# Performance work log

Hardware: AMD Instinct MI355X
Metric: run time of the kernel (lower is better)

Reference implementation:

```python
import jax, jax.numpy as jnp
import numpy as np

D_MODEL = 1024
N_HEADS = 16
D_K = D_MODEL // N_HEADS
D_FF = 4096
EPS = 1e-6


def setup_inputs() -> dict:
    key = jax.random.key(0)
    ks = jax.random.split(key, 12)
    s = 1.0 / np.sqrt(D_MODEL)
    inp = {
        "x": jax.random.normal(ks[0], (4, 2048, D_MODEL), jnp.float32),
        "src_mask": jnp.ones((4, 1, 1, 2048), jnp.int32),
        "Wq": jax.random.normal(ks[1], (D_MODEL, D_MODEL), jnp.float32) * s,
        "bq": jnp.zeros((D_MODEL,), jnp.float32),
        "Wk": jax.random.normal(ks[2], (D_MODEL, D_MODEL), jnp.float32) * s,
        "bk": jnp.zeros((D_MODEL,), jnp.float32),
        "Wv": jax.random.normal(ks[3], (D_MODEL, D_MODEL), jnp.float32) * s,
        "bv": jnp.zeros((D_MODEL,), jnp.float32),
        "Wo": jax.random.normal(ks[4], (D_MODEL, D_MODEL), jnp.float32) * s,
        "bo": jnp.zeros((D_MODEL,), jnp.float32),
        "W1": jax.random.normal(ks[5], (D_MODEL, D_FF), jnp.float32) * s,
        "b1": jnp.zeros((D_FF,), jnp.float32),
        "W2": jax.random.normal(ks[6], (D_FF, D_MODEL), jnp.float32) * (1.0 / np.sqrt(D_FF)),
        "b2": jnp.zeros((D_MODEL,), jnp.float32),
        # scalar LayerNormalization params (alpha=ones(1), bias=zeros(1)) for the 2 residual norms
        "ln1_alpha": jnp.ones((1,), jnp.float32),
        "ln1_bias": jnp.zeros((1,), jnp.float32),
        "ln2_alpha": jnp.ones((1,), jnp.float32),
        "ln2_bias": jnp.zeros((1,), jnp.float32),
    }
    return inp


def _layernorm(x, alpha, bias):
    # matches torch: mean + std (unbiased, ddof=1), (x-mean)/(std+eps)
    mean = jnp.mean(x, axis=-1, keepdims=True)
    std = jnp.std(x, axis=-1, keepdims=True, ddof=1)
    return alpha * ((x - mean) / (std + EPS)) + bias


def _mha(x, mask, Wq, bq, Wk, bk, Wv, bv, Wo, bo):
    B, S, _ = x.shape
    q = (x @ Wq + bq).reshape(B, S, N_HEADS, D_K).transpose(0, 2, 1, 3)
    k = (x @ Wk + bk).reshape(B, S, N_HEADS, D_K).transpose(0, 2, 1, 3)
    v = (x @ Wv + bv).reshape(B, S, N_HEADS, D_K).transpose(0, 2, 1, 3)
    scores = jnp.einsum("bhqd,bhkd->bhqk", q, k) / jnp.sqrt(jnp.float32(D_K))
    scores = jnp.where(mask == 0, jnp.float32(-1e9), scores)
    attn = jax.nn.softmax(scores, axis=-1)
    ctx = jnp.einsum("bhqk,bhkd->bhqd", attn, v)
    ctx = ctx.transpose(0, 2, 1, 3).reshape(B, S, D_MODEL)
    return ctx @ Wo + bo


def reference(x, src_mask, Wq, bq, Wk, bk, Wv, bv, Wo, bo, W1, b1, W2, b2,
              ln1_alpha, ln1_bias, ln2_alpha, ln2_bias):
    # pre-norm residual 1: self-attention
    h = _layernorm(x, ln1_alpha, ln1_bias)
    x = x + _mha(h, src_mask, Wq, bq, Wk, bk, Wv, bv, Wo, bo)
    # pre-norm residual 2: FFN
    h = _layernorm(x, ln2_alpha, ln2_bias)
    ff = jax.nn.relu(h @ W1 + b1) @ W2 + b2
    return x + ff
```

## Files before the change

### kernel.cpp

```cpp
#include <hip/hip_runtime.h>

typedef __attribute__((ext_vector_type(8))) short v8s;
typedef __attribute__((ext_vector_type(8))) unsigned short v8u;
typedef __attribute__((ext_vector_type(4))) unsigned short v4u;
typedef __attribute__((ext_vector_type(4))) float f32x4;

#define DEV __device__ __forceinline__

DEV unsigned short f2bf(float f) {
  union { float f; unsigned u; } v; v.f = f;
  unsigned r = v.u + 0x7fffu + ((v.u >> 16) & 1u);
  return (unsigned short)(r >> 16);
}

DEV float bf2f(unsigned short s) {
  union { unsigned u; float f; } v; v.u = ((unsigned)s) << 16; return v.f;
}

DEV float fexp2(float x) {
  float r; asm("v_exp_f32 %0, %1" : "=v"(r) : "v"(x)); return r;
}

DEV void gload16(const unsigned short* g, unsigned short* l) {
  __builtin_amdgcn_global_load_lds(
      (const __attribute__((address_space(1))) unsigned int*)g,
      (__attribute__((address_space(3))) unsigned int*)l, 16, 0, 0);
}

#define SL2E 0.1803368801111204f

__global__ __launch_bounds__(256) void ln_kernel(
    const float* __restrict__ x, unsigned short* __restrict__ h,
    const float* __restrict__ alpha, const float* __restrict__ beta)
{
  int row = blockIdx.x;
  int tid = threadIdx.x;
  const float4* xr = reinterpret_cast<const float4*>(x + (size_t)row * 1024);
  float4 v = xr[tid];
  float s  = v.x + v.y + v.z + v.w;
  float ss = v.x * v.x + v.y * v.y + v.z * v.z + v.w * v.w;
#pragma unroll
  for (int off = 1; off < 64; off <<= 1) {
    s  += __shfl_xor(s, off);
    ss += __shfl_xor(ss, off);
  }
  __shared__ float ps[4][2];
  int wid = tid >> 6, lane = tid & 63;
  if (lane == 0) { ps[wid][0] = s; ps[wid][1] = ss; }
  __syncthreads();
  s  = ps[0][0] + ps[1][0] + ps[2][0] + ps[3][0];
  ss = ps[0][1] + ps[1][1] + ps[2][1] + ps[3][1];
  float mean = s * (1.0f / 1024.0f);
  float var  = (ss - 1024.0f * mean * mean) * (1.0f / 1023.0f);
  float inv  = 1.0f / (sqrtf(fmaxf(var, 0.0f)) + 1e-6f);
  float a = alpha[0], b = beta[0];
  v4u o;
  o[0] = f2bf(a * ((v.x - mean) * inv) + b);
  o[1] = f2bf(a * ((v.y - mean) * inv) + b);
  o[2] = f2bf(a * ((v.z - mean) * inv) + b);
  o[3] = f2bf(a * ((v.w - mean) * inv) + b);
  *reinterpret_cast<v4u*>(h + (size_t)row * 1024 + tid * 4) = o;
}

__global__ __launch_bounds__(256) void transpose_convert(
    const float* __restrict__ W, unsigned short* __restrict__ Wt, int K, int N)
{
  __shared__ float t[32][33];
  int n0 = blockIdx.x * 32, k0 = blockIdx.y * 32;
  int tx = threadIdx.x, ty = threadIdx.y;
#pragma unroll
  for (int i = 0; i < 4; ++i)
    t[ty + i * 8][tx] = W[(size_t)(k0 + ty + i * 8) * N + n0 + tx];
  __syncthreads();
#pragma unroll
  for (int i = 0; i < 4; ++i)
    Wt[(size_t)(n0 + ty + i * 8) * K + k0 + tx] = f2bf(t[tx][ty + i * 8]);
}

enum { MODE_QKV = 0, MODE_FFN1 = 3, MODE_PART = 4 };

template <int MODE>
__global__ __launch_bounds__(512, 1) void gemm_256s(
    const unsigned short* __restrict__ A, const unsigned short* __restrict__ Bt,
    const float* __restrict__ bias0, const float* __restrict__ bias1,
    const float* __restrict__ bias2,
    void* __restrict__ o0, void* __restrict__ o1, void* __restrict__ o2,
    int M, int N, int K, int KRUN)
{
  __shared__ unsigned short lds[2][512 * 64];

  int nbx = M >> 8, nwg = gridDim.x;
  int lin = blockIdx.x;
  int qq = nwg >> 3, rr = nwg & 7;
  int xcd = lin & 7, idx = lin >> 3;
  int swz = (xcd < rr ? xcd * (qq + 1) : rr * (qq + 1) + (xcd - rr) * qq) + idx;

  int bx, by, kbase;
  if constexpr (MODE == MODE_PART) {
    int h = swz >> 7, s2 = swz & 127;
    bx = s2 % nbx; by = s2 / nbx; kbase = h * KRUN;
  } else {
    bx = swz % nbx; by = swz / nbx; kbase = 0;
  }

  int tid = threadIdx.x, lane = tid & 63, wid = tid >> 6;
  int wm = wid >> 2, wn = wid & 3;
  int g = lane >> 4, c0 = lane & 15;
  int rowBase = bx * 256, colBase = by * 256;

  const unsigned short* Ab = A  + (size_t)rowBase * K + kbase;
  const unsigned short* Bb = Bt + (size_t)colBase * K + kbase;
  int NT = KRUN >> 6;

  const unsigned short* src[8]; int dq[8];
#pragma unroll
  for (int i = 0; i < 8; ++i) {
    int q = i * 512 + tid;
    dq[i] = q;
    if (i < 4) {
      int r = q >> 3, p = q & 7;
      src[i] = Ab + (size_t)r * K + 8 * (p ^ (r & 7));
    } else {
      int qb2 = q - 2048, r = qb2 >> 3, p = qb2 & 7;
      src[i] = Bb + (size_t)r * K + 8 * (p ^ (r & 7));
    }
  }

  f32x4 acc[8][4];
#pragma unroll
  for (int m = 0; m < 8; ++m)
#pragma unroll
    for (int n = 0; n < 4; ++n) acc[m][n] = (f32x4){0.f, 0.f, 0.f, 0.f};

#define STG256(tt, lo, hi) do { \
    unsigned short* sb_ = &lds[(tt) & 1][0]; int ko_ = (tt) << 6; \
    _Pragma("unroll") for (int i = lo; i < hi; ++i) gload16(src[i] + ko_, sb_ + dq[i] * 8); \
  } while (0)

  STG256(0, 0, 8);
  asm volatile("s_waitcnt vmcnt(0)" ::: "memory");
  __builtin_amdgcn_s_barrier();
  asm volatile("" ::: "memory");

  for (int t = 0; t < NT; ++t) {
    const char* buf = (const char*)&lds[t & 1][0];
    bool more = (t + 1 < NT);

#pragma unroll
    for (int ph = 0; ph < 2; ++ph) {
      v8s af[8], bfr[4];
#pragma unroll
      for (int m = 0; m < 8; ++m) {
        int row = wm * 128 + m * 16 + c0;
        af[m] = *reinterpret_cast<const v8s*>(
            buf + row * 128 + ((ph * 64 + g * 16) ^ ((row & 7) << 4)));
      }
#pragma unroll
      for (int n = 0; n < 4; ++n) {
        int row = wn * 64 + n * 16 + c0;
        bfr[n] = *reinterpret_cast<const v8s*>(
            buf + 32768 + row * 128 + ((ph * 64 + g * 16) ^ ((row & 7) << 4)));
      }

      if (more) { if (ph == 0) STG256(t + 1, 0, 4); else STG256(t + 1, 4, 8); }

      __builtin_amdgcn_s_setprio(1);
#pragma unroll
      for (int m = 0; m < 8; ++m)
#pragma unroll
        for (int n = 0; n < 4; ++n)
          acc[m][n] = __builtin_amdgcn_mfma_f32_16x16x32_bf16(
              af[m], bfr[n], acc[m][n], 0, 0, 0);
      __builtin_amdgcn_s_setprio(0);
    }

    if (more) asm volatile("s_waitcnt vmcnt(0)" ::: "memory");
    __builtin_amdgcn_sched_barrier(0);
    __builtin_amdgcn_s_barrier();
    asm volatile("" ::: "memory");
  }
#undef STG256

#pragma unroll
  for (int mf = 0; mf < 8; ++mf) {
#pragma unroll
    for (int nf = 0; nf < 4; ++nf) {
#pragma unroll
      for (int r = 0; r < 4; ++r) {
        int row = rowBase + wm * 128 + mf * 16 + g * 4 + r;
        int col = colBase + wn * 64 + nf * 16 + c0;
        float v = acc[mf][nf][r];
        if constexpr (MODE == MODE_QKV) {
          int sect = colBase >> 10;
          int cs = col & 1023;
          const float* bp = sect == 0 ? bias0 : (sect == 1 ? bias1 : bias2);
          v += bp[cs];
          int hh = cs >> 6, d = cs & 63;
          int b = row >> 11, sI = row & 2047;
          size_t bh = (size_t)(b * 16 + hh);
          if (sect == 0) {
            ((unsigned short*)o0)[(bh * 2048 + sI) * 64 + d] = f2bf(v * SL2E);
          } else if (sect == 1) {
            ((unsigned short*)o1)[(bh * 2048 + sI) * 64 + d] = f2bf(v);
          } else {
            int k6 = sI & 63;
            int slot = ((k6 >> 5) << 5) | (((k6 >> 2) & 3) << 3) |
                       (((k6 >> 4) & 1) << 2) | (k6 & 3);
            int e2 = slot ^ ((d & 7) << 3);
            ((unsigned short*)o2)[((bh * 32 + (sI >> 6)) * 64 + d) * 64 + e2] = f2bf(v);
          }
        } else if constexpr (MODE == MODE_FFN1) {
          v += bias0[col];
          ((unsigned short*)o0)[(size_t)row * N + col] = f2bf(fmaxf(v, 0.0f));
        } else {
          unsigned short* po = (kbase == 0) ? (unsigned short*)o0 : (unsigned short*)o1;
          po[(size_t)row * N + col] = f2bf(v);
        }
      }
    }
  }
}

__global__ __launch_bounds__(256) void ffn2_combine(
    const unsigned short* __restrict__ p0, const unsigned short* __restrict__ p1,
    const float* __restrict__ b2, float* __restrict__ xout)
{
  size_t off = ((size_t)blockIdx.x * 256 + threadIdx.x) * 4;
  int col = (int)(off & 1023);
  float4 xv = *reinterpret_cast<const float4*>(xout + off);
  v4u a = *reinterpret_cast<const v4u*>(p0 + off);
  v4u b = *reinterpret_cast<const v4u*>(p1 + off);
  float4 bb = *reinterpret_cast<const float4*>(b2 + col);
  float4 o;
  o.x = xv.x + bb.x + bf2f(a[0]) + bf2f(b[0]);
  o.y = xv.y + bb.y + bf2f(a[1]) + bf2f(b[1]);
  o.z = xv.z + bb.z + bf2f(a[2]) + bf2f(b[2]);
  o.w = xv.w + bb.w + bf2f(a[3]) + bf2f(b[3]);
  *reinterpret_cast<float4*>(xout + off) = o;
}

#define BUF_ELEMS ((128 + 256) * 64)

DEV void stage_part(const unsigned short* Aptr, const unsigned short* Bptr,
                    unsigned short* buf, int K, int part, int wid, int lane)
{
  {
    int d = (part * 8 + wid) * 64 + lane;
    int r = d >> 3, p = d & 7;
    gload16(Aptr + (size_t)r * K + 8 * (p ^ (r & 7)),
            buf + (size_t)(part * 8 + wid) * 512);
  }
#pragma unroll
  for (int j = 0; j < 2; ++j) {
    int ib = part * 2 + j;
    int d = (ib * 8 + wid) * 64 + lane;
    int r = d >> 3, p = d & 7;
    gload16(Bptr + (size_t)r * K + 8 * (p ^ (r & 7)),
            buf + 128 * 64 + (size_t)(ib * 8 + wid) * 512);
  }
}

__global__ __launch_bounds__(512, 1) void gemm_pipe_res(
    const unsigned short* __restrict__ A, const unsigned short* __restrict__ Bt,
    const float* __restrict__ bias0, const float* __restrict__ resid,
    float* __restrict__ o0, int M, int N, int K)
{
  __shared__ unsigned short lds[3 * BUF_ELEMS];

  int nbx = M >> 7, nwg = gridDim.x;
  int lin = blockIdx.x;
  int qq = nwg >> 3, rr = nwg & 7;
  int xcd = lin & 7, idx = lin >> 3;
  int swz = (xcd < rr ? xcd * (qq + 1) : rr * (qq + 1) + (xcd - rr) * qq) + idx;
  int bx = swz % nbx, by = swz / nbx;

  int tid = threadIdx.x, lane = tid & 63, wid = tid >> 6;
  int g = lane >> 4, c0 = lane & 15;
  int rowBase = bx * 128, colBase = by * 256;

  const unsigned short* Ab = A  + (size_t)rowBase * K;
  const unsigned short* Bb = Bt + (size_t)colBase * K;
  int NT = K >> 6;

  f32x4 acc[8][2];
#pragma unroll
  for (int m = 0; m < 8; ++m)
#pragma unroll
    for (int n = 0; n < 2; ++n) acc[m][n] = (f32x4){0.f, 0.f, 0.f, 0.f};

  stage_part(Ab, Bb, lds, K, 0, wid, lane);
  stage_part(Ab, Bb, lds, K, 1, wid, lane);
  stage_part(Ab + 64, Bb + 64, lds + BUF_ELEMS, K, 0, wid, lane);
  stage_part(Ab + 64, Bb + 64, lds + BUF_ELEMS, K, 1, wid, lane);
  asm volatile("s_waitcnt vmcnt(6)" ::: "memory");
  __builtin_amdgcn_s_barrier();
  asm volatile("" ::: "memory");

  int cur = 0;
  for (int t = 0; t < NT; ++t) {
    const char* Abuf = (const char*)(lds + cur * BUF_ELEMS);
    const char* Bbuf = Abuf + 128 * 128;
    int nxt2 = cur + 2; if (nxt2 >= 3) nxt2 -= 3;
    unsigned short* sbuf = lds + nxt2 * BUF_ELEMS;
    bool doStage = (t + 2 < NT);
    int ks_ = (t + 2) << 6;

#pragma unroll
    for (int ph = 0; ph < 2; ++ph) {
      v8s af[8], bfr[2];
#pragma unroll
      for (int m = 0; m < 8; ++m) {
        int row = m * 16 + c0;
        af[m] = *reinterpret_cast<const v8s*>(
            Abuf + row * 128 + ((ph * 64 + g * 16) ^ ((row & 7) << 4)));
      }
#pragma unroll
      for (int n = 0; n < 2; ++n) {
        int row = wid * 32 + n * 16 + c0;
        bfr[n] = *reinterpret_cast<const v8s*>(
            Bbuf + row * 128 + ((ph * 64 + g * 16) ^ ((row & 7) << 4)));
      }

      if (doStage) stage_part(Ab + ks_, Bb + ks_, sbuf, K, ph, wid, lane);

      __builtin_amdgcn_s_setprio(1);
#pragma unroll
      for (int m = 0; m < 8; ++m)
#pragma unroll
        for (int n = 0; n < 2; ++n)
          acc[m][n] = __builtin_amdgcn_mfma_f32_16x16x32_bf16(
              af[m], bfr[n], acc[m][n], 0, 0, 0);
      __builtin_amdgcn_s_setprio(0);
    }

    if (doStage)            asm volatile("s_waitcnt vmcnt(6)" ::: "memory");
    else if (t + 1 < NT)    asm volatile("s_waitcnt vmcnt(0)" ::: "memory");
    __builtin_amdgcn_sched_barrier(0);
    __builtin_amdgcn_s_barrier();
    asm volatile("" ::: "memory");
    cur = cur + 1; if (cur >= 3) cur -= 3;
  }

#pragma unroll
  for (int mf = 0; mf < 8; ++mf) {
#pragma unroll
    for (int nf = 0; nf < 2; ++nf) {
#pragma unroll
      for (int r = 0; r < 4; ++r) {
        int row = rowBase + mf * 16 + g * 4 + r;
        int col = colBase + wid * 32 + nf * 16 + c0;
        float v = acc[mf][nf][r] + bias0[col];
        o0[(size_t)row * N + col] = resid[(size_t)row * N + col] + v;
      }
    }
  }
}

__global__ __launch_bounds__(256, 2) void attn_kernel(
    const unsigned short* __restrict__ q, const unsigned short* __restrict__ k,
    const unsigned short* __restrict__ vP, const int* __restrict__ mask,
    unsigned short* __restrict__ ctx)
{
  const int S = 2048, DK = 64, NT = 32;
  int bh = blockIdx.x;
  int b = bh >> 4, hh = bh & 15;
  int qbase = blockIdx.y * 256;
  int tid = threadIdx.x, lane = tid & 63, wid = tid >> 6;
  int g = lane >> 4, c0 = lane & 15;

  __shared__ unsigned short Ks[3 * 4096];
  __shared__ unsigned short Vs[3 * 4096];
  __shared__ unsigned short Mb[2048];

  const unsigned short* qb  = q  + (size_t)bh * S * DK;
  const unsigned short* kb  = k  + (size_t)bh * S * DK;
  const unsigned short* vPb = vP + (size_t)bh * 32 * 4096;
  const int* mb = mask + b * S;

  const int4* mb4 = reinterpret_cast<const int4*>(mb);
  int4 ma = mb4[tid * 2], mc = mb4[tid * 2 + 1];
  unsigned short bneg = f2bf(-1e9f);
  v8u bw;
  bw[0] = ma.x ? 0 : bneg; bw[1] = ma.y ? 0 : bneg;
  bw[2] = ma.z ? 0 : bneg; bw[3] = ma.w ? 0 : bneg;
  bw[4] = mc.x ? 0 : bneg; bw[5] = mc.y ? 0 : bneg;
  bw[6] = mc.z ? 0 : bneg; bw[7] = mc.w ? 0 : bneg;
  *reinterpret_cast<v8u*>(&Mb[tid * 8]) = bw;
  int okm = (ma.x && ma.y && ma.z && ma.w && mc.x && mc.y && mc.z && mc.w) ? 1 : 0;
  int allValid = __syncthreads_and(okm);

  int qrow = qbase + wid * 64 + c0;
  v8s aq[4][2];
#pragma unroll
  for (int s = 0; s < 4; ++s)
#pragma unroll
    for (int t = 0; t < 2; ++t)
      aq[s][t] = *reinterpret_cast<const v8s*>(
          &qb[(size_t)(qrow + s * 16) * DK + t * 32 + g * 8]);

  int i0 = tid, i1 = tid + 256;
  int r0 = i0 >> 3, m0 = i0 & 7;
  int r1 = i1 >> 3, m1 = i1 & 7;
  int ko0 = r0 * DK + 8 * (m0 ^ (r0 & 7));
  int ko1 = r1 * DK + 8 * (m1 ^ (r1 & 7));

  f32x4 acc[4][4], accl[4];
#pragma unroll
  for (int s = 0; s < 4; ++s) {
    accl[s] = (f32x4){0.f, 0.f, 0.f, 0.f};
#pragma unroll
    for (int no = 0; no < 4; ++no) acc[s][no] = (f32x4){0.f, 0.f, 0.f, 0.f};
  }
  v8s ones;
#pragma unroll
  for (int j = 0; j < 8; ++j) ones[j] = (short)0x3F80;

#define ASTAGE(bi, tt) do { \
    int tb_ = (tt) * 4096; \
    gload16(kb + tb_ + ko0, Ks + (bi) * 4096 + i0 * 8); \
    gload16(kb + tb_ + ko1, Ks + (bi) * 4096 + i1 * 8); \
    gload16(vPb + tb_ + i0 * 8, Vs + (bi) * 4096 + i0 * 8); \
    gload16(vPb + tb_ + i1 * 8, Vs + (bi) * 4096 + i1 * 8); \
  } while (0)

  ASTAGE(0, 0);
  ASTAGE(1, 1);
  asm volatile("s_waitcnt vmcnt(4)" ::: "memory");
  __builtin_amdgcn_s_barrier();
  asm volatile("" ::: "memory");

  int cur = 0, nx2 = 2;
  for (int t = 0; t < NT; ++t) {
    bool more2 = (t + 2 < NT);
    if (more2) ASTAGE(nx2, t + 2);
    const unsigned short* Kc = Ks + cur * 4096;
    const unsigned short* Vc = Vs + cur * 4096;

    v8s pb[4][2];
#pragma unroll
    for (int pp = 0; pp < 2; ++pp) {
      float pA[16], pB[16];
#pragma unroll
      for (int n = 0; n < 4; ++n) {
        int kvr = n * 16 + c0;
        const char* krow = (const char*)(Kc + kvr * DK);
        int sw = (kvr & 7) << 4;
        v8s ak0 = *reinterpret_cast<const v8s*>(krow + ((g * 16) ^ sw));
        v8s ak1 = *reinterpret_cast<const v8s*>(krow + ((64 + g * 16) ^ sw));
        f32x4 s0 = (f32x4){0.f, 0.f, 0.f, 0.f};
        f32x4 s1 = (f32x4){0.f, 0.f, 0.f, 0.f};
        s0 = __builtin_amdgcn_mfma_f32_16x16x32_bf16(ak0, aq[pp * 2][0], s0, 0, 0, 0);
        s0 = __builtin_amdgcn_mfma_f32_16x16x32_bf16(ak1, aq[pp * 2][1], s0, 0, 0, 0);
        s1 = __builtin_amdgcn_mfma_f32_16x16x32_bf16(ak0, aq[pp * 2 + 1][0], s1, 0, 0, 0);
        s1 = __builtin_amdgcn_mfma_f32_16x16x32_bf16(ak1, aq[pp * 2 + 1][1], s1, 0, 0, 0);
#pragma unroll
        for (int r = 0; r < 4; ++r) { pA[n * 4 + r] = s0[r]; pB[n * 4 + r] = s1[r]; }
      }
      if (!allValid) {
#pragma unroll
        for (int n = 0; n < 4; ++n) {
          v4u mbv = *reinterpret_cast<const v4u*>(&Mb[t * 64 + n * 16 + g * 4]);
#pragma unroll
          for (int r = 0; r < 4; ++r) {
            union { unsigned u; float f; } cv; cv.u = ((unsigned)mbv[r]) << 16;
            pA[n * 4 + r] += cv.f; pB[n * 4 + r] += cv.f;
          }
        }
      }
#pragma unroll
      for (int i = 0; i < 16; ++i) { pA[i] = fexp2(pA[i]); pB[i] = fexp2(pB[i]); }
#pragma unroll
      for (int c = 0; c < 2; ++c) {
        union { v8s s; unsigned u[4]; } kA, kB;
#pragma unroll
        for (int hp = 0; hp < 4; ++hp) {
          asm("v_cvt_pk_bf16_f32 %0, %1, %2"
              : "=v"(kA.u[hp]) : "v"(pA[c * 8 + 2 * hp]), "v"(pA[c * 8 + 2 * hp + 1]));
          asm("v_cvt_pk_bf16_f32 %0, %1, %2"
              : "=v"(kB.u[hp]) : "v"(pB[c * 8 + 2 * hp]), "v"(pB[c * 8 + 2 * hp + 1]));
        }
        pb[pp * 2][c] = kA.s; pb[pp * 2 + 1][c] = kB.s;
      }
    }

    __builtin_amdgcn_s_setprio(1);
#pragma unroll
    for (int c = 0; c < 2; ++c) {
#pragma unroll
      for (int no = 0; no < 4; ++no) {
        int d = no * 16 + c0;
        v8s av = *reinterpret_cast<const v8s*>(
            (const char*)(Vc + d * 64) + ((c * 64 + g * 16) ^ ((d & 7) << 4)));
#pragma unroll
        for (int s = 0; s < 4; ++s)
          acc[s][no] = __builtin_amdgcn_mfma_f32_16x16x32_bf16(av, pb[s][c], acc[s][no], 0, 0, 0);
      }
#pragma unroll
      for (int s = 0; s < 4; ++s)
        accl[s] = __builtin_amdgcn_mfma_f32_16x16x32_bf16(ones, pb[s][c], accl[s], 0, 0, 0);
    }
    __builtin_amdgcn_s_setprio(0);

    if (more2)              asm volatile("s_waitcnt vmcnt(4)" ::: "memory");
    else if (t + 1 < NT)    asm volatile("s_waitcnt vmcnt(0)" ::: "memory");
    __builtin_amdgcn_sched_barrier(0);
    __builtin_amdgcn_s_barrier();
    asm volatile("" ::: "memory");
    cur = (cur + 1 < 3) ? cur + 1 : 0;
    nx2 = (nx2 + 1 < 3) ? nx2 + 1 : 0;
  }
#undef ASTAGE

#pragma unroll
  for (int s = 0; s < 4; ++s) {
    float inv = 1.0f / fmaxf(accl[s][0], 1e-30f);
#pragma unroll
    for (int no = 0; no < 4; ++no) {
      v4u o;
      o[0] = f2bf(acc[s][no][0] * inv);
      o[1] = f2bf(acc[s][no][1] * inv);
      o[2] = f2bf(acc[s][no][2] * inv);
      o[3] = f2bf(acc[s][no][3] * inv);
      *reinterpret_cast<v4u*>(
          &ctx[(size_t)(b * S + qrow + s * 16) * 1024 + hh * 64 + no * 16 + g * 4]) = o;
    }
  }
}

extern "C" void kernel_launch(void* const* d_in, const int* in_sizes, int n_in,
                              void* d_out, int out_size, void* d_ws, size_t ws_size,
                              hipStream_t stream)
{
  (void)in_sizes; (void)n_in; (void)out_size; (void)ws_size;
  const float* x    = (const float*)d_in[0];
  const int*   mask = (const int*)d_in[1];
  const float* Wq = (const float*)d_in[2];  const float* bq = (const float*)d_in[3];
  const float* Wk = (const float*)d_in[4];  const float* bk = (const float*)d_in[5];
  const float* Wv = (const float*)d_in[6];  const float* bv = (const float*)d_in[7];
  const float* Wo = (const float*)d_in[8];  const float* bo = (const float*)d_in[9];
  const float* W1 = (const float*)d_in[10]; const float* b1 = (const float*)d_in[11];
  const float* W2 = (const float*)d_in[12]; const float* b2 = (const float*)d_in[13];
  const float* ln1a = (const float*)d_in[14]; const float* ln1b = (const float*)d_in[15];
  const float* ln2a = (const float*)d_in[16]; const float* ln2b = (const float*)d_in[17];

  char* ws = (char*)d_ws;
  const size_t MB = (size_t)1 << 20;
  unsigned short* wqkvT = (unsigned short*)(ws + 0 * MB);
  unsigned short* p1  = (unsigned short*)(ws + 0 * MB);
  unsigned short* woT = (unsigned short*)(ws + 6 * MB);
  unsigned short* w1T = (unsigned short*)(ws + 8 * MB);
  unsigned short* w2T = (unsigned short*)(ws + 16 * MB);
  unsigned short* hb  = (unsigned short*)(ws + 24 * MB);
  unsigned short* p0  = (unsigned short*)(ws + 24 * MB);
  unsigned short* qb  = (unsigned short*)(ws + 40 * MB);
  unsigned short* kb  = (unsigned short*)(ws + 56 * MB);
  unsigned short* vPb = (unsigned short*)(ws + 72 * MB);
  unsigned short* ctx = (unsigned short*)(ws + 88 * MB);
  unsigned short* gb  = (unsigned short*)(ws + 40 * MB);
  float* xout = (float*)d_out;

  dim3 tb(32, 8);
  transpose_convert<<<dim3(32, 32),  tb, 0, stream>>>(Wq, wqkvT,               1024, 1024);
  transpose_convert<<<dim3(32, 32),  tb, 0, stream>>>(Wk, wqkvT + 1024 * 1024, 1024, 1024);
  transpose_convert<<<dim3(32, 32),  tb, 0, stream>>>(Wv, wqkvT + 2048 * 1024, 1024, 1024);
  transpose_convert<<<dim3(32, 32),  tb, 0, stream>>>(Wo, woT, 1024, 1024);
  transpose_convert<<<dim3(128, 32), tb, 0, stream>>>(W1, w1T, 1024, 4096);
  transpose_convert<<<dim3(32, 128), tb, 0, stream>>>(W2, w2T, 4096, 1024);

  ln_kernel<<<8192, 256, 0, stream>>>(x, hb, ln1a, ln1b);

  gemm_256s<MODE_QKV><<<384, 512, 0, stream>>>(
      hb, wqkvT, bq, bk, bv, qb, kb, vPb, 8192, 3072, 1024, 1024);

  attn_kernel<<<dim3(64, 8), 256, 0, stream>>>(qb, kb, vPb, mask, ctx);

  gemm_pipe_res<<<256, 512, 0, stream>>>(ctx, woT, bo, x, xout, 8192, 1024, 1024);

  ln_kernel<<<8192, 256, 0, stream>>>(xout, hb, ln2a, ln2b);

  gemm_256s<MODE_FFN1><<<512, 512, 0, stream>>>(
      hb, w1T, b1, nullptr, nullptr, gb, nullptr, nullptr, 8192, 4096, 1024, 1024);

  gemm_256s<MODE_PART><<<256, 512, 0, stream>>>(
      gb, w2T, nullptr, nullptr, nullptr, p0, p1, nullptr, 8192, 1024, 4096, 2048);

  ffn2_combine<<<8192, 256, 0, stream>>>(p0, p1, b2, xout);
}
```

Baseline: 386.4 us.

## Use 128x128 double-buffered GEMM for QKV, out-proj and unsplit FFN2 with fused residual

Adds a 256-thread, 128x128-tile double-buffered GEMM that runs two workgroups per CU. It now handles the QKV projection, the output projection and FFN2. FFN2 no longer splits K into two bf16 partial outputs plus a separate combine kernel; bias and residual are added in its epilogue, which removes one launch and the partial-result traffic. The trade-off is smaller tiles, hence less data reuse per workgroup, and fewer workgroups for FFN2 with a longer K loop.

```diff
diff --git a/kernel.cpp b/kernel.cpp
--- a/kernel.cpp
+++ b/kernel.cpp
@@ -11,10 +11,6 @@
   union { float f; unsigned u; } v; v.f = f;
   unsigned r = v.u + 0x7fffu + ((v.u >> 16) & 1u);
   return (unsigned short)(r >> 16);
-}
-
-DEV float bf2f(unsigned short s) {
-  union { unsigned u; float f; } v; v.u = ((unsigned)s) << 16; return v.f;
 }
 
 DEV float fexp2(float x) {
@@ -77,67 +73,60 @@
     Wt[(size_t)(n0 + ty + i * 8) * K + k0 + tx] = f2bf(t[tx][ty + i * 8]);
 }
 
-enum { MODE_QKV = 0, MODE_FFN1 = 3, MODE_PART = 4 };
+enum { MODE_QKV = 0, MODE_RES = 2 };
 
 template <int MODE>
-__global__ __launch_bounds__(512, 1) void gemm_256s(
+__global__ __launch_bounds__(256, 2) void gemm_dbuf(
     const unsigned short* __restrict__ A, const unsigned short* __restrict__ Bt,
     const float* __restrict__ bias0, const float* __restrict__ bias1,
-    const float* __restrict__ bias2,
+    const float* __restrict__ bias2, const float* __restrict__ resid,
     void* __restrict__ o0, void* __restrict__ o1, void* __restrict__ o2,
-    int M, int N, int K, int KRUN)
+    int M, int N, int K)
 {
-  __shared__ unsigned short lds[2][512 * 64];
-
-  int nbx = M >> 8, nwg = gridDim.x;
+  __shared__ unsigned short lds[2][2 * 128 * 64];
+
+  int nbx = M >> 7, nwg = gridDim.x;
   int lin = blockIdx.x;
   int qq = nwg >> 3, rr = nwg & 7;
   int xcd = lin & 7, idx = lin >> 3;
   int swz = (xcd < rr ? xcd * (qq + 1) : rr * (qq + 1) + (xcd - rr) * qq) + idx;
-
-  int bx, by, kbase;
-  if constexpr (MODE == MODE_PART) {
-    int h = swz >> 7, s2 = swz & 127;
-    bx = s2 % nbx; by = s2 / nbx; kbase = h * KRUN;
-  } else {
-    bx = swz % nbx; by = swz / nbx; kbase = 0;
-  }
+  int bx = swz % nbx, by = swz / nbx;
 
   int tid = threadIdx.x, lane = tid & 63, wid = tid >> 6;
-  int wm = wid >> 2, wn = wid & 3;
+  int wm = wid >> 1, wn = wid & 1;
   int g = lane >> 4, c0 = lane & 15;
-  int rowBase = bx * 256, colBase = by * 256;
-
-  const unsigned short* Ab = A  + (size_t)rowBase * K + kbase;
-  const unsigned short* Bb = Bt + (size_t)colBase * K + kbase;
-  int NT = KRUN >> 6;
+  int rowBase = bx * 128, colBase = by * 128;
+
+  const unsigned short* Ab = A  + (size_t)rowBase * K;
+  const unsigned short* Bb = Bt + (size_t)colBase * K;
+  int NT = K >> 6;
 
   const unsigned short* src[8]; int dq[8];
 #pragma unroll
   for (int i = 0; i < 8; ++i) {
-    int q = i * 512 + tid;
-    dq[i] = q;
+    int q = (i & 3) * 256 + tid;
+    int r = q >> 3, p = q & 7;
     if (i < 4) {
-      int r = q >> 3, p = q & 7;
       src[i] = Ab + (size_t)r * K + 8 * (p ^ (r & 7));
+      dq[i] = q * 8;
     } else {
-      int qb2 = q - 2048, r = qb2 >> 3, p = qb2 & 7;
       src[i] = Bb + (size_t)r * K + 8 * (p ^ (r & 7));
-    }
-  }
-
-  f32x4 acc[8][4];
-#pragma unroll
-  for (int m = 0; m < 8; ++m)
+      dq[i] = 8192 + q * 8;
+    }
+  }
+
+  f32x4 acc[4][4];
+#pragma unroll
+  for (int m = 0; m < 4; ++m)
 #pragma unroll
     for (int n = 0; n < 4; ++n) acc[m][n] = (f32x4){0.f, 0.f, 0.f, 0.f};
 
-#define STG256(tt, lo, hi) do { \
+#define STGD(tt, lo, hi) do { \
     unsigned short* sb_ = &lds[(tt) & 1][0]; int ko_ = (tt) << 6; \
-    _Pragma("unroll") for (int i = lo; i < hi; ++i) gload16(src[i] + ko_, sb_ + dq[i] * 8); \
+    _Pragma("unroll") for (int i = lo; i < hi; ++i) gload16(src[i] + ko_, sb_ + dq[i]); \
   } while (0)
 
-  STG256(0, 0, 8);
+  STGD(0, 0, 8);
   asm volatile("s_waitcnt vmcnt(0)" ::: "memory");
   __builtin_amdgcn_s_barrier();
   asm volatile("" ::: "memory");
@@ -148,10 +137,10 @@
 
 #pragma unroll
     for (int ph = 0; ph < 2; ++ph) {
-      v8s af[8], bfr[4];
-#pragma unroll
-      for (int m = 0; m < 8; ++m) {
-        int row = wm * 128 + m * 16 + c0;
+      v8s af[4], bfr[4];
+#pragma unroll
+      for (int m = 0; m < 4; ++m) {
+        int row = wm * 64 + m * 16 + c0;
         af[m] = *reinterpret_cast<const v8s*>(
             buf + row * 128 + ((ph * 64 + g * 16) ^ ((row & 7) << 4)));
       }
@@ -159,14 +148,14 @@
       for (int n = 0; n < 4; ++n) {
         int row = wn * 64 + n * 16 + c0;
         bfr[n] = *reinterpret_cast<const v8s*>(
-            buf + 32768 + row * 128 + ((ph * 64 + g * 16) ^ ((row & 7) << 4)));
-      }
-
-      if (more) { if (ph == 0) STG256(t + 1, 0, 4); else STG256(t + 1, 4, 8); }
+            buf + 16384 + row * 128 + ((ph * 64 + g * 16) ^ ((row & 7) << 4)));
+      }
+
+      if (more) { if (ph == 0) STGD(t + 1, 0, 4); else STGD(t + 1, 4, 8); }
 
       __builtin_amdgcn_s_setprio(1);
 #pragma unroll
-      for (int m = 0; m < 8; ++m)
+      for (int m = 0; m < 4; ++m)
 #pragma unroll
         for (int n = 0; n < 4; ++n)
           acc[m][n] = __builtin_amdgcn_mfma_f32_16x16x32_bf16(
@@ -179,15 +168,15 @@
     __builtin_amdgcn_s_barrier();
     asm volatile("" ::: "memory");
   }
-#undef STG256
-
-#pragma unroll
-  for (int mf = 0; mf < 8; ++mf) {
+#undef STGD
+
+#pragma unroll
+  for (int mf = 0; mf < 4; ++mf) {
 #pragma unroll
     for (int nf = 0; nf < 4; ++nf) {
 #pragma unroll
       for (int r = 0; r < 4; ++r) {
-        int row = rowBase + wm * 128 + mf * 16 + g * 4 + r;
+        int row = rowBase + wm * 64 + mf * 16 + g * 4 + r;
         int col = colBase + wn * 64 + nf * 16 + c0;
         float v = acc[mf][nf][r];
         if constexpr (MODE == MODE_QKV) {
@@ -209,65 +198,24 @@
             int e2 = slot ^ ((d & 7) << 3);
             ((unsigned short*)o2)[((bh * 32 + (sI >> 6)) * 64 + d) * 64 + e2] = f2bf(v);
           }
-        } else if constexpr (MODE == MODE_FFN1) {
+        } else {
           v += bias0[col];
-          ((unsigned short*)o0)[(size_t)row * N + col] = f2bf(fmaxf(v, 0.0f));
-        } else {
-          unsigned short* po = (kbase == 0) ? (unsigned short*)o0 : (unsigned short*)o1;
-          po[(size_t)row * N + col] = f2bf(v);
+          ((float*)o0)[(size_t)row * N + col] =
+              resid[(size_t)row * N + col] + v;
         }
       }
     }
   }
 }
 
-__global__ __launch_bounds__(256) void ffn2_combine(
-    const unsigned short* __restrict__ p0, const unsigned short* __restrict__ p1,
-    const float* __restrict__ b2, float* __restrict__ xout)
+__global__ __launch_bounds__(512, 1) void gemm_ffn1_256(
+    const unsigned short* __restrict__ A, const unsigned short* __restrict__ Bt,
+    const float* __restrict__ bias, unsigned short* __restrict__ out,
+    int M, int N, int K)
 {
-  size_t off = ((size_t)blockIdx.x * 256 + threadIdx.x) * 4;
-  int col = (int)(off & 1023);
-  float4 xv = *reinterpret_cast<const float4*>(xout + off);
-  v4u a = *reinterpret_cast<const v4u*>(p0 + off);
-  v4u b = *reinterpret_cast<const v4u*>(p1 + off);
-  float4 bb = *reinterpret_cast<const float4*>(b2 + col);
-  float4 o;
-  o.x = xv.x + bb.x + bf2f(a[0]) + bf2f(b[0]);
-  o.y = xv.y + bb.y + bf2f(a[1]) + bf2f(b[1]);
-  o.z = xv.z + bb.z + bf2f(a[2]) + bf2f(b[2]);
-  o.w = xv.w + bb.w + bf2f(a[3]) + bf2f(b[3]);
-  *reinterpret_cast<float4*>(xout + off) = o;
-}
-
-#define BUF_ELEMS ((128 + 256) * 64)
-
-DEV void stage_part(const unsigned short* Aptr, const unsigned short* Bptr,
-                    unsigned short* buf, int K, int part, int wid, int lane)
-{
-  {
-    int d = (part * 8 + wid) * 64 + lane;
-    int r = d >> 3, p = d & 7;
-    gload16(Aptr + (size_t)r * K + 8 * (p ^ (r & 7)),
-            buf + (size_t)(part * 8 + wid) * 512);
-  }
-#pragma unroll
-  for (int j = 0; j < 2; ++j) {
-    int ib = part * 2 + j;
-    int d = (ib * 8 + wid) * 64 + lane;
-    int r = d >> 3, p = d & 7;
-    gload16(Bptr + (size_t)r * K + 8 * (p ^ (r & 7)),
-            buf + 128 * 64 + (size_t)(ib * 8 + wid) * 512);
-  }
-}
-
-__global__ __launch_bounds__(512, 1) void gemm_pipe_res(
-    const unsigned short* __restrict__ A, const unsigned short* __restrict__ Bt,
-    const float* __restrict__ bias0, const float* __restrict__ resid,
-    float* __restrict__ o0, int M, int N, int K)
-{
-  __shared__ unsigned short lds[3 * BUF_ELEMS];
-
-  int nbx = M >> 7, nwg = gridDim.x;
+  __shared__ unsigned short lds[2][512 * 64];
+
+  int nbx = M >> 8, nwg = gridDim.x;
   int lin = blockIdx.x;
   int qq = nwg >> 3, rr = nwg & 7;
   int xcd = lin & 7, idx = lin >> 3;
@@ -275,82 +223,93 @@
   int bx = swz % nbx, by = swz / nbx;
 
   int tid = threadIdx.x, lane = tid & 63, wid = tid >> 6;
+  int wm = wid >> 2, wn = wid & 3;
   int g = lane >> 4, c0 = lane & 15;
-  int rowBase = bx * 128, colBase = by * 256;
+  int rowBase = bx * 256, colBase = by * 256;
 
   const unsigned short* Ab = A  + (size_t)rowBase * K;
   const unsigned short* Bb = Bt + (size_t)colBase * K;
   int NT = K >> 6;
 
-  f32x4 acc[8][2];
+  const unsigned short* src[8]; int dq[8];
+#pragma unroll
+  for (int i = 0; i < 8; ++i) {
+    int q = i * 512 + tid;
+    dq[i] = q;
+    if (i < 4) {
+      int r = q >> 3, p = q & 7;
+      src[i] = Ab + (size_t)r * K + 8 * (p ^ (r & 7));
+    } else {
+      int qb2 = q - 2048, r = qb2 >> 3, p = qb2 & 7;
+      src[i] = Bb + (size_t)r * K + 8 * (p ^ (r & 7));
+    }
+  }
+
+  f32x4 acc[8][4];
 #pragma unroll
   for (int m = 0; m < 8; ++m)
 #pragma unroll
-    for (int n = 0; n < 2; ++n) acc[m][n] = (f32x4){0.f, 0.f, 0.f, 0.f};
-
-  stage_part(Ab, Bb, lds, K, 0, wid, lane);
-  stage_part(Ab, Bb, lds, K, 1, wid, lane);
-  stage_part(Ab + 64, Bb + 64, lds + BUF_ELEMS, K, 0, wid, lane);
-  stage_part(Ab + 64, Bb + 64, lds + BUF_ELEMS, K, 1, wid, lane);
-  asm volatile("s_waitcnt vmcnt(6)" ::: "memory");
+    for (int n = 0; n < 4; ++n) acc[m][n] = (f32x4){0.f, 0.f, 0.f, 0.f};
+
+#define STG256(tt, lo, hi) do { \
+    unsigned short* sb_ = &lds[(tt) & 1][0]; int ko_ = (tt) << 6; \
+    _Pragma("unroll") for (int i = lo; i < hi; ++i) gload16(src[i] + ko_, sb_ + dq[i] * 8); \
+  } while (0)
+
+  STG256(0, 0, 8);
+  asm volatile("s_waitcnt vmcnt(0)" ::: "memory");
   __builtin_amdgcn_s_barrier();
   asm volatile("" ::: "memory");
 
-  int cur = 0;
   for (int t = 0; t < NT; ++t) {
-    const char* Abuf = (const char*)(lds + cur * BUF_ELEMS);
-    const char* Bbuf = Abuf + 128 * 128;
-    int nxt2 = cur + 2; if (nxt2 >= 3) nxt2 -= 3;
-    unsigned short* sbuf = lds + nxt2 * BUF_ELEMS;
-    bool doStage = (t + 2 < NT);
-    int ks_ = (t + 2) << 6;
+    const char* buf = (const char*)&lds[t & 1][0];
+    bool more = (t + 1 < NT);
 
 #pragma unroll
     for (int ph = 0; ph < 2; ++ph) {
-      v8s af[8], bfr[2];
+      v8s af[8], bfr[4];
 #pragma unroll
       for (int m = 0; m < 8; ++m) {
-        int row = m * 16 + c0;
+        int row = wm * 128 + m * 16 + c0;
         af[m] = *reinterpret_cast<const v8s*>(
-            Abuf + row * 128 + ((ph * 64 + g * 16) ^ ((row & 7) << 4)));
-      }
-#pragma unroll
-      for (int n = 0; n < 2; ++n) {
-        int row = wid * 32 + n * 16 + c0;
+            buf + row * 128 + ((ph * 64 + g * 16) ^ ((row & 7) << 4)));
+      }
+#pragma unroll
+      for (int n = 0; n < 4; ++n) {
+        int row = wn * 64 + n * 16 + c0;
         bfr[n] = *reinterpret_cast<const v8s*>(
-            Bbuf + row * 128 + ((ph * 64 + g * 16) ^ ((row & 7) << 4)));
-      }
-
-      if (doStage) stage_part(Ab + ks_, Bb + ks_, sbuf, K, ph, wid, lane);
+            buf + 32768 + row * 128 + ((ph * 64 + g * 16) ^ ((row & 7) << 4)));
+      }
+
+      if (more) { if (ph == 0) STG256(t + 1, 0, 4); else STG256(t + 1, 4, 8); }
 
       __builtin_amdgcn_s_setprio(1);
 #pragma unroll
       for (int m = 0; m < 8; ++m)
 #pragma unroll
-        for (int n = 0; n < 2; ++n)
+        for (int n = 0; n < 4; ++n)
           acc[m][n] = __builtin_amdgcn_mfma_f32_16x16x32_bf16(
               af[m], bfr[n], acc[m][n], 0, 0, 0);
       __builtin_amdgcn_s_setprio(0);
     }
 
-    if (doStage)            asm volatile("s_waitcnt vmcnt(6)" ::: "memory");
-    else if (t + 1 < NT)    asm volatile("s_waitcnt vmcnt(0)" ::: "memory");
+    if (more) asm volatile("s_waitcnt vmcnt(0)" ::: "memory");
     __builtin_amdgcn_sched_barrier(0);
     __builtin_amdgcn_s_barrier();
     asm volatile("" ::: "memory");
-    cur = cur + 1; if (cur >= 3) cur -= 3;
-  }
+  }
+#undef STG256
 
 #pragma unroll
   for (int mf = 0; mf < 8; ++mf) {
 #pragma unroll
-    for (int nf = 0; nf < 2; ++nf) {
+    for (int nf = 0; nf < 4; ++nf) {
 #pragma unroll
       for (int r = 0; r < 4; ++r) {
-        int row = rowBase + mf * 16 + g * 4 + r;
-        int col = colBase + wid * 32 + nf * 16 + c0;
-        float v = acc[mf][nf][r] + bias0[col];
-        o0[(size_t)row * N + col] = resid[(size_t)row * N + col] + v;
+        int row = rowBase + wm * 128 + mf * 16 + g * 4 + r;
+        int col = colBase + wn * 64 + nf * 16 + c0;
+        float v = acc[mf][nf][r] + bias[col];
+        out[(size_t)row * N + col] = f2bf(fmaxf(v, 0.0f));
       }
     }
   }
@@ -546,12 +505,10 @@
   char* ws = (char*)d_ws;
   const size_t MB = (size_t)1 << 20;
   unsigned short* wqkvT = (unsigned short*)(ws + 0 * MB);
-  unsigned short* p1  = (unsigned short*)(ws + 0 * MB);
   unsigned short* woT = (unsigned short*)(ws + 6 * MB);
   unsigned short* w1T = (unsigned short*)(ws + 8 * MB);
   unsigned short* w2T = (unsigned short*)(ws + 16 * MB);
   unsigned short* hb  = (unsigned short*)(ws + 24 * MB);
-  unsigned short* p0  = (unsigned short*)(ws + 24 * MB);
   unsigned short* qb  = (unsigned short*)(ws + 40 * MB);
   unsigned short* kb  = (unsigned short*)(ws + 56 * MB);
   unsigned short* vPb = (unsigned short*)(ws + 72 * MB);
@@ -569,20 +526,18 @@
 
   ln_kernel<<<8192, 256, 0, stream>>>(x, hb, ln1a, ln1b);
 
-  gemm_256s<MODE_QKV><<<384, 512, 0, stream>>>(
-      hb, wqkvT, bq, bk, bv, qb, kb, vPb, 8192, 3072, 1024, 1024);
+  gemm_dbuf<MODE_QKV><<<1536, 256, 0, stream>>>(
+      hb, wqkvT, bq, bk, bv, nullptr, qb, kb, vPb, 8192, 3072, 1024);
 
   attn_kernel<<<dim3(64, 8), 256, 0, stream>>>(qb, kb, vPb, mask, ctx);
 
-  gemm_pipe_res<<<256, 512, 0, stream>>>(ctx, woT, bo, x, xout, 8192, 1024, 1024);
+  gemm_dbuf<MODE_RES><<<512, 256, 0, stream>>>(
+      ctx, woT, bo, nullptr, nullptr, x, xout, nullptr, nullptr, 8192, 1024, 1024);
 
   ln_kernel<<<8192, 256, 0, stream>>>(xout, hb, ln2a, ln2b);
 
-  gemm_256s<MODE_FFN1><<<512, 512, 0, stream>>>(
-      hb, w1T, b1, nullptr, nullptr, gb, nullptr, nullptr, 8192, 4096, 1024, 1024);
-
-  gemm_256s<MODE_PART><<<256, 512, 0, stream>>>(
-      gb, w2T, nullptr, nullptr, nullptr, p0, p1, nullptr, 8192, 1024, 4096, 2048);
-
-  ffn2_combine<<<8192, 256, 0, stream>>>(p0, p1, b2, xout);
-}
+  gemm_ffn1_256<<<512, 512, 0, stream>>>(hb, w1T, b1, gb, 8192, 4096, 1024);
+
+  gemm_dbuf<MODE_RES><<<512, 256, 0, stream>>>(
+      gb, w2T, b2, nullptr, nullptr, xout, xout, nullptr, nullptr, 8192, 1024, 4096);
+}
```

Result: no change. 386.4 us (+0.0%).
